# Optimization experiments

Hardware: AMD Instinct MI355X
Metric: run time of the kernel (lower is better)

## Reference

```python
import jax, jax.numpy as jnp
import numpy as np

C = 4  # n_features_per_level
RES = [128, 256, 512, 1024]  # base_resolution=128, per_level_scale=2, n_levels=4


def grid_sample(grid, pts):
    """Bilinear grid_sample, align_corners=False, zero padding.
    grid: (B, C, H, W); pts: (B, N, 2) with pts[...,0]=x (width), pts[...,1]=y (height).
    Returns (B, C, N)."""
    B, Cc, H, W = grid.shape
    fx = (pts[..., 0] + 1.0) * 0.5 * W - 0.5
    fy = (pts[..., 1] + 1.0) * 0.5 * H - 0.5
    x0 = jnp.floor(fx)
    y0 = jnp.floor(fy)
    wx = (fx - x0)[:, None, :]
    wy = (fy - y0)[:, None, :]
    x0 = x0.astype(jnp.int32)
    y0 = y0.astype(jnp.int32)

    def corner(xi, yi):
        valid = ((xi >= 0) & (xi < W) & (yi >= 0) & (yi < H)).astype(grid.dtype)
        xc = jnp.clip(xi, 0, W - 1)
        yc = jnp.clip(yi, 0, H - 1)
        vals = jax.vmap(lambda g, yy, xx: g[:, yy, xx])(grid, yc, xc)  # (B, C, N)
        return vals * valid[:, None, :]

    v00 = corner(x0, y0)
    v10 = corner(x0 + 1, y0)
    v01 = corner(x0, y0 + 1)
    v11 = corner(x0 + 1, y0 + 1)
    return (v00 * (1 - wx) * (1 - wy) + v10 * wx * (1 - wy)
            + v01 * (1 - wx) * wy + v11 * wx * wy)


def _flat(f):
    # (3, C, N) -> (N, 3*C), matching torch out.reshape(3*C, N).T
    return f.reshape(3 * f.shape[1], f.shape[2]).T


def _forward(x, triplanes, trilines):
    x2 = x * 2.0 - 1.0  # map [0,1] -> [-1,1]
    # plane projections: (xz), (yx), (zy)
    x_pl = jnp.stack([
        jnp.stack([x2[:, 0], x2[:, 2]], -1),
        jnp.stack([x2[:, 1], x2[:, 0]], -1),
        jnp.stack([x2[:, 2], x2[:, 1]], -1)], 0)  # (3, N, 2)
    x_li = jnp.stack([x2[:, 0], x2[:, 1], x2[:, 2]], 0)
    x_li = jnp.stack([x_li, jnp.zeros_like(x_li)], -1)  # (3, N, 2)
    feats = []
    for tp, tl in zip(triplanes, trilines):
        f = _flat(grid_sample(tp, x_pl)) * _flat(grid_sample(tl, x_li))  # (N, 3C)
        feats.append(f)
    return jnp.concatenate(feats, -1)  # (N, 3*C*n_levels)


def setup_inputs() -> dict:
    key = jax.random.key(0)
    ks = jax.random.split(key, 9)
    N = 1 << 20
    d = {"x": jax.random.uniform(ks[0], (N, 3), jnp.float32)}
    for i, r in enumerate(RES):
        d[f"triplane_{i}"] = jax.random.normal(ks[1 + i], (3, C, r, r), jnp.float32)
        d[f"triline_{i}"] = jax.random.normal(ks[5 + i], (3, C, r, 1), jnp.float32)
    return d


def reference(x, triplane_0, triplane_1, triplane_2, triplane_3,
              triline_0, triline_1, triline_2, triline_3):
    triplanes = [triplane_0, triplane_1, triplane_2, triplane_3]
    trilines = [triline_0, triline_1, triline_2, triline_3]
    return _forward(x, triplanes, trilines)
```

## Files before the change

kernel.cpp:

```cpp
#include <hip/hip_runtime.h>
#include <cstdint>


static constexpr int LVL_OFF[4] = {0, 196608, 983040, 4128768};
static constexpr int S_OFF = 16711680;
static constexpr size_t WS_NEED = (size_t)(S_OFF + 48) * sizeof(float);

__global__ __launch_bounds__(256) void repack_lvl(const float* __restrict__ src,
                                                  float* __restrict__ dst,
                                                  int rr_shift ) {
    int j = blockIdx.x * blockDim.x + threadIdx.x;
    int c  = j & 3;
    int t  = j >> 2;
    int p  = t >> rr_shift;
    int yx = t & ((1 << rr_shift) - 1);
    dst[j] = src[(((size_t)(p * 4 + c)) << rr_shift) + yx];
}

__global__ void line_consts(const float* __restrict__ tl0, const float* __restrict__ tl1,
                            const float* __restrict__ tl2, const float* __restrict__ tl3,
                            float* __restrict__ s_out) {
    int i = threadIdx.x;
    if (i >= 48) return;
    int l = i / 12, rem = i % 12, p = rem >> 2, c = rem & 3;
    const float* tl = (l == 0) ? tl0 : (l == 1) ? tl1 : (l == 2) ? tl2 : tl3;
    int r = 128 << l;
    const float* row = tl + (size_t)((p << 2) + c) * r;
    int y0 = (r >> 1) - 1;
    s_out[i] = 0.5f * row[y0] + 0.5f * row[y0 + 1];
}

struct BilinW {
    int i00, i10, i01, i11;
    float w00, w10, w01, w11;
};

__device__ __forceinline__ BilinW bilin_weights(int r, float u, float v) {
    float fr = (float)r;
    float fx = (u + 1.0f) * 0.5f * fr - 0.5f;
    float fy = (v + 1.0f) * 0.5f * fr - 0.5f;
    float x0f = floorf(fx), y0f = floorf(fy);
    float wx = fx - x0f, wy = fy - y0f;
    int x0 = (int)x0f, y0 = (int)y0f;
    int x1 = x0 + 1, y1 = y0 + 1;
    float vx0 = ((unsigned)x0 < (unsigned)r) ? 1.0f : 0.0f;
    float vx1 = ((unsigned)x1 < (unsigned)r) ? 1.0f : 0.0f;
    float vy0 = ((unsigned)y0 < (unsigned)r) ? 1.0f : 0.0f;
    float vy1 = ((unsigned)y1 < (unsigned)r) ? 1.0f : 0.0f;
    int x0c = min(max(x0, 0), r - 1), x1c = min(max(x1, 0), r - 1);
    int y0c = min(max(y0, 0), r - 1), y1c = min(max(y1, 0), r - 1);
    BilinW b;
    b.i00 = y0c * r + x0c; b.i10 = y0c * r + x1c;
    b.i01 = y1c * r + x0c; b.i11 = y1c * r + x1c;
    b.w00 = (1.0f - wx) * (1.0f - wy) * vx0 * vy0;
    b.w10 = wx * (1.0f - wy) * vx1 * vy0;
    b.w01 = (1.0f - wx) * wy * vx0 * vy1;
    b.w11 = wx * wy * vx1 * vy1;
    return b;
}

__device__ __forceinline__ float line_w(float t) {
    float fx = (t + 1.0f) * 0.5f - 0.5f;
    float x0f = floorf(fx);
    float wx = fx - x0f;
    int x0 = (int)x0f;
    float w = 0.0f;
    if (x0 == 0) w += 1.0f - wx;
    if (x0 == -1) w += wx;
    return w;
}

template <bool VEC4OUT>
__global__ __launch_bounds__(256) void tri_main(const float* __restrict__ x,
                                                const float4* __restrict__ planes,
                                                const float* __restrict__ S,
                                                float* __restrict__ out, int N) {
    int n = blockIdx.x * blockDim.x + threadIdx.x;
    if (n >= N) return;
    float ax = x[n * 3 + 0] * 2.0f - 1.0f;
    float ay = x[n * 3 + 1] * 2.0f - 1.0f;
    float az = x[n * 3 + 2] * 2.0f - 1.0f;
    const float U[3] = {ax, ay, az};
    const float V[3] = {az, ax, ay};
    const float LW[3] = {line_w(ax), line_w(ay), line_w(az)};

#pragma unroll
    for (int l = 0; l < 4; ++l) {
        const int r = 128 << l;
#pragma unroll
        for (int p = 0; p < 3; ++p) {
            const float4* G = planes + (LVL_OFF[l] >> 2) + (size_t)p * r * r;
            BilinW b = bilin_weights(r, U[p], V[p]);
            float4 g00 = G[b.i00], g10 = G[b.i10], g01 = G[b.i01], g11 = G[b.i11];
            float w = LW[p];
            float sx = S[(l * 3 + p) * 4 + 0] * w;
            float sy = S[(l * 3 + p) * 4 + 1] * w;
            float sz = S[(l * 3 + p) * 4 + 2] * w;
            float sw = S[(l * 3 + p) * 4 + 3] * w;
            float4 o;
            o.x = (g00.x * b.w00 + g10.x * b.w10 + g01.x * b.w01 + g11.x * b.w11) * sx;
            o.y = (g00.y * b.w00 + g10.y * b.w10 + g01.y * b.w01 + g11.y * b.w11) * sy;
            o.z = (g00.z * b.w00 + g10.z * b.w10 + g01.z * b.w01 + g11.z * b.w11) * sz;
            o.w = (g00.w * b.w00 + g10.w * b.w10 + g01.w * b.w01 + g11.w * b.w11) * sw;
            size_t base = (size_t)n * 48 + (size_t)(l * 12 + p * 4);
            if (VEC4OUT) {
                *reinterpret_cast<float4*>(out + base) = o;
            } else {
                out[base + 0] = o.x; out[base + 1] = o.y;
                out[base + 2] = o.z; out[base + 3] = o.w;
            }
        }
    }
}

__global__ __launch_bounds__(256) void tri_direct(
        const float* __restrict__ x,
        const float* __restrict__ tp0, const float* __restrict__ tp1,
        const float* __restrict__ tp2, const float* __restrict__ tp3,
        const float* __restrict__ tl0, const float* __restrict__ tl1,
        const float* __restrict__ tl2, const float* __restrict__ tl3,
        float* __restrict__ out, int N) {
    int n = blockIdx.x * blockDim.x + threadIdx.x;
    if (n >= N) return;
    float ax = x[n * 3 + 0] * 2.0f - 1.0f;
    float ay = x[n * 3 + 1] * 2.0f - 1.0f;
    float az = x[n * 3 + 2] * 2.0f - 1.0f;
    const float U[3] = {ax, ay, az};
    const float V[3] = {az, ax, ay};
    const float LW[3] = {line_w(ax), line_w(ay), line_w(az)};
    const float* TP[4] = {tp0, tp1, tp2, tp3};
    const float* TL[4] = {tl0, tl1, tl2, tl3};

#pragma unroll
    for (int l = 0; l < 4; ++l) {
        const int r = 128 << l;
        const int rr = r * r;
        const int y0 = (r >> 1) - 1;
#pragma unroll
        for (int p = 0; p < 3; ++p) {
            const float* G = TP[l] + (size_t)(p * 4) * rr;
            BilinW b = bilin_weights(r, U[p], V[p]);
            const float w = LW[p];
#pragma unroll
            for (int c = 0; c < 4; ++c) {
                const float* Gc = G + (size_t)c * rr;
                float acc = Gc[b.i00] * b.w00 + Gc[b.i10] * b.w10 +
                            Gc[b.i01] * b.w01 + Gc[b.i11] * b.w11;
                const float* row = TL[l] + (size_t)((p << 2) + c) * r;
                float s = 0.5f * row[y0] + 0.5f * row[y0 + 1];
                out[(size_t)n * 48 + l * 12 + p * 4 + c] = acc * (s * w);
            }
        }
    }
}

extern "C" void kernel_launch(void* const* d_in, const int* in_sizes, int n_in,
                              void* d_out, int out_size, void* d_ws, size_t ws_size,
                              hipStream_t stream) {
    const float* x = (const float*)d_in[0];
    const float* tp[4];
    const float* tl[4];
    bool interleaved = (n_in >= 9) && (in_sizes[2] == 1536);
    for (int l = 0; l < 4; ++l) {
        if (interleaved) {
            tp[l] = (const float*)d_in[1 + 2 * l];
            tl[l] = (const float*)d_in[2 + 2 * l];
        } else {
            tp[l] = (const float*)d_in[1 + l];
            tl[l] = (const float*)d_in[5 + l];
        }
    }
    int N = in_sizes[0] / 3;
    float* out = (float*)d_out;
    int grid = (N + 255) / 256;

    bool ws_ok = (ws_size >= WS_NEED) && (((uintptr_t)d_ws & 15u) == 0);
    if (ws_ok) {
        float* ws = (float*)d_ws;
        for (int l = 0; l < 4; ++l) {
            int r = 128 << l;
            int total = 12 * r * r;
            int rr_shift = 2 * (7 + l);
            repack_lvl<<<total / 256, 256, 0, stream>>>(tp[l], ws + LVL_OFF[l], rr_shift);
        }
        line_consts<<<1, 64, 0, stream>>>(tl[0], tl[1], tl[2], tl[3], ws + S_OFF);
        if (((uintptr_t)d_out & 15u) == 0) {
            tri_main<true><<<grid, 256, 0, stream>>>(x, (const float4*)ws, ws + S_OFF, out, N);
        } else {
            tri_main<false><<<grid, 256, 0, stream>>>(x, (const float4*)ws, ws + S_OFF, out, N);
        }
    } else {
        tri_direct<<<grid, 256, 0, stream>>>(
            x, tp[0], tp[1], tp[2], tp[3], tl[0], tl[1], tl[2], tl[3], out, N);
    }
}
```

Measured before the change: 660.4 us.

## Merge repack kernels and split per-point work across four level threads

Replaces the four per-level repack launches and the line-constant kernel with a single repack_all kernel. Each thread of that kernel gathers four channels and writes one float4. The main kernel now assigns one thread per (point, level) pair instead of one per point. Each thread issues all 12 plane gathers up front and writes its 48 output bytes with nontemporal vector stores, which should give more memory-level parallelism and fewer launches. In exchange, every thread recomputes the input load and line weights, and the grid is four times larger.

```diff
diff --git a/kernel.cpp b/kernel.cpp
--- a/kernel.cpp
+++ b/kernel.cpp
@@ -1,33 +1,44 @@
 #include <hip/hip_runtime.h>
 #include <cstdint>
 
+
+typedef float f32x4 __attribute__((ext_vector_type(4)));
 
 static constexpr int LVL_OFF[4] = {0, 196608, 983040, 4128768};
 static constexpr int S_OFF = 16711680;
 static constexpr size_t WS_NEED = (size_t)(S_OFF + 48) * sizeof(float);
-
-__global__ __launch_bounds__(256) void repack_lvl(const float* __restrict__ src,
-                                                  float* __restrict__ dst,
-                                                  int rr_shift ) {
-    int j = blockIdx.x * blockDim.x + threadIdx.x;
-    int c  = j & 3;
-    int t  = j >> 2;
-    int p  = t >> rr_shift;
-    int yx = t & ((1 << rr_shift) - 1);
-    dst[j] = src[(((size_t)(p * 4 + c)) << rr_shift) + yx];
-}
-
-__global__ void line_consts(const float* __restrict__ tl0, const float* __restrict__ tl1,
-                            const float* __restrict__ tl2, const float* __restrict__ tl3,
-                            float* __restrict__ s_out) {
-    int i = threadIdx.x;
-    if (i >= 48) return;
-    int l = i / 12, rem = i % 12, p = rem >> 2, c = rem & 3;
-    const float* tl = (l == 0) ? tl0 : (l == 1) ? tl1 : (l == 2) ? tl2 : tl3;
-    int r = 128 << l;
-    const float* row = tl + (size_t)((p << 2) + c) * r;
-    int y0 = (r >> 1) - 1;
-    s_out[i] = 0.5f * row[y0] + 0.5f * row[y0 + 1];
+static constexpr int TEXELS = 4177920;
+
+__global__ __launch_bounds__(256) void repack_all(
+        const float* __restrict__ tp0, const float* __restrict__ tp1,
+        const float* __restrict__ tp2, const float* __restrict__ tp3,
+        const float* __restrict__ tl0, const float* __restrict__ tl1,
+        const float* __restrict__ tl2, const float* __restrict__ tl3,
+        float* __restrict__ ws) {
+    int t = blockIdx.x * 256 + threadIdx.x;
+    const float* src; int rr_shift, texoff;
+    if (t < 49152)        { src = tp0; rr_shift = 14; texoff = 0; }
+    else if (t < 245760)  { src = tp1; rr_shift = 16; texoff = 49152; }
+    else if (t < 1032192) { src = tp2; rr_shift = 18; texoff = 245760; }
+    else                  { src = tp3; rr_shift = 20; texoff = 1032192; }
+    int local = t - texoff;
+    int p  = local >> rr_shift;
+    int yx = local & ((1 << rr_shift) - 1);
+    const float* s0 = src + ((size_t)(p << 2) << rr_shift) + yx;
+    float4 o;
+    o.x = s0[0];
+    o.y = s0[(size_t)1 << rr_shift];
+    o.z = s0[(size_t)2 << rr_shift];
+    o.w = s0[(size_t)3 << rr_shift];
+    reinterpret_cast<float4*>(ws)[t] = o;
+    if (t < 48) {
+        int ll = t / 12, rem = t % 12, pp = rem >> 2, cc = rem & 3;
+        const float* tl = (ll == 0) ? tl0 : (ll == 1) ? tl1 : (ll == 2) ? tl2 : tl3;
+        int r = 128 << ll;
+        const float* row = tl + (size_t)((pp << 2) + cc) * r;
+        int y0 = (r >> 1) - 1;
+        ws[S_OFF + t] = 0.5f * row[y0] + 0.5f * row[y0 + 1];
+    }
 }
 
 struct BilinW {
@@ -70,46 +81,61 @@
     return w;
 }
 
+__device__ __forceinline__ f32x4 bacc(const float4& A, const float4& B2,
+                                      const float4& C2, const float4& D,
+                                      const BilinW& b, const float4& s, float lw) {
+    f32x4 o;
+    o.x = (A.x * b.w00 + B2.x * b.w10 + C2.x * b.w01 + D.x * b.w11) * (s.x * lw);
+    o.y = (A.y * b.w00 + B2.y * b.w10 + C2.y * b.w01 + D.y * b.w11) * (s.y * lw);
+    o.z = (A.z * b.w00 + B2.z * b.w10 + C2.z * b.w01 + D.z * b.w11) * (s.z * lw);
+    o.w = (A.w * b.w00 + B2.w * b.w10 + C2.w * b.w01 + D.w * b.w11) * (s.w * lw);
+    return o;
+}
+
 template <bool VEC4OUT>
-__global__ __launch_bounds__(256) void tri_main(const float* __restrict__ x,
-                                                const float4* __restrict__ planes,
-                                                const float* __restrict__ S,
-                                                float* __restrict__ out, int N) {
-    int n = blockIdx.x * blockDim.x + threadIdx.x;
+__global__ __launch_bounds__(256, 2) void tri_split4(
+        const float* __restrict__ x, const float4* __restrict__ planes,
+        const float* __restrict__ S, float* __restrict__ out, int N) {
+    int gid = blockIdx.x * 256 + threadIdx.x;
+    int n = gid >> 2;
+    int l = gid & 3;
     if (n >= N) return;
     float ax = x[n * 3 + 0] * 2.0f - 1.0f;
     float ay = x[n * 3 + 1] * 2.0f - 1.0f;
     float az = x[n * 3 + 2] * 2.0f - 1.0f;
-    const float U[3] = {ax, ay, az};
-    const float V[3] = {az, ax, ay};
-    const float LW[3] = {line_w(ax), line_w(ay), line_w(az)};
-
-#pragma unroll
-    for (int l = 0; l < 4; ++l) {
-        const int r = 128 << l;
-#pragma unroll
-        for (int p = 0; p < 3; ++p) {
-            const float4* G = planes + (LVL_OFF[l] >> 2) + (size_t)p * r * r;
-            BilinW b = bilin_weights(r, U[p], V[p]);
-            float4 g00 = G[b.i00], g10 = G[b.i10], g01 = G[b.i01], g11 = G[b.i11];
-            float w = LW[p];
-            float sx = S[(l * 3 + p) * 4 + 0] * w;
-            float sy = S[(l * 3 + p) * 4 + 1] * w;
-            float sz = S[(l * 3 + p) * 4 + 2] * w;
-            float sw = S[(l * 3 + p) * 4 + 3] * w;
-            float4 o;
-            o.x = (g00.x * b.w00 + g10.x * b.w10 + g01.x * b.w01 + g11.x * b.w11) * sx;
-            o.y = (g00.y * b.w00 + g10.y * b.w10 + g01.y * b.w01 + g11.y * b.w11) * sy;
-            o.z = (g00.z * b.w00 + g10.z * b.w10 + g01.z * b.w01 + g11.z * b.w11) * sz;
-            o.w = (g00.w * b.w00 + g10.w * b.w10 + g01.w * b.w01 + g11.w * b.w11) * sw;
-            size_t base = (size_t)n * 48 + (size_t)(l * 12 + p * 4);
-            if (VEC4OUT) {
-                *reinterpret_cast<float4*>(out + base) = o;
-            } else {
-                out[base + 0] = o.x; out[base + 1] = o.y;
-                out[base + 2] = o.z; out[base + 3] = o.w;
-            }
-        }
+    const int r = 128 << l;
+    const int rr = r * r;
+    int texoff = (l == 0) ? 0 : (l == 1) ? 49152 : (l == 2) ? 245760 : 1032192;
+    const float4* G0 = planes + texoff;
+    const float4* G1 = G0 + rr;
+    const float4* G2 = G1 + rr;
+    BilinW b0 = bilin_weights(r, ax, az);
+    BilinW b1 = bilin_weights(r, ay, ax);
+    BilinW b2 = bilin_weights(r, az, ay);
+    float4 g0a = G0[b0.i00], g0b = G0[b0.i10], g0c = G0[b0.i01], g0d = G0[b0.i11];
+    float4 g1a = G1[b1.i00], g1b = G1[b1.i10], g1c = G1[b1.i01], g1d = G1[b1.i11];
+    float4 g2a = G2[b2.i00], g2b = G2[b2.i10], g2c = G2[b2.i01], g2d = G2[b2.i11];
+    float lw0 = line_w(ax), lw1 = line_w(ay), lw2 = line_w(az);
+    const float4* S4 = reinterpret_cast<const float4*>(S);
+    float4 s0 = S4[l * 3 + 0], s1 = S4[l * 3 + 1], s2 = S4[l * 3 + 2];
+
+    f32x4 o0 = bacc(g0a, g0b, g0c, g0d, b0, s0, lw0);
+    f32x4 o1 = bacc(g1a, g1b, g1c, g1d, b1, s1, lw1);
+    f32x4 o2 = bacc(g2a, g2b, g2c, g2d, b2, s2, lw2);
+
+    size_t base = (size_t)n * 48 + (size_t)l * 12;
+    if (VEC4OUT) {
+        f32x4* op = reinterpret_cast<f32x4*>(out + base);
+        __builtin_nontemporal_store(o0, op);
+        __builtin_nontemporal_store(o1, op + 1);
+        __builtin_nontemporal_store(o2, op + 2);
+    } else {
+        out[base + 0] = o0.x; out[base + 1]  = o0.y;
+        out[base + 2] = o0.z; out[base + 3]  = o0.w;
+        out[base + 4] = o1.x; out[base + 5]  = o1.y;
+        out[base + 6] = o1.z; out[base + 7]  = o1.w;
+        out[base + 8] = o2.x; out[base + 9]  = o2.y;
+        out[base + 10] = o2.z; out[base + 11] = o2.w;
     }
 }
 
@@ -172,24 +198,23 @@
     }
     int N = in_sizes[0] / 3;
     float* out = (float*)d_out;
-    int grid = (N + 255) / 256;
 
     bool ws_ok = (ws_size >= WS_NEED) && (((uintptr_t)d_ws & 15u) == 0);
     if (ws_ok) {
         float* ws = (float*)d_ws;
-        for (int l = 0; l < 4; ++l) {
-            int r = 128 << l;
-            int total = 12 * r * r;
-            int rr_shift = 2 * (7 + l);
-            repack_lvl<<<total / 256, 256, 0, stream>>>(tp[l], ws + LVL_OFF[l], rr_shift);
-        }
-        line_consts<<<1, 64, 0, stream>>>(tl[0], tl[1], tl[2], tl[3], ws + S_OFF);
+        repack_all<<<TEXELS / 256, 256, 0, stream>>>(
+            tp[0], tp[1], tp[2], tp[3], tl[0], tl[1], tl[2], tl[3], ws);
+        long long total = 4LL * N;
+        int grid = (int)((total + 255) / 256);
         if (((uintptr_t)d_out & 15u) == 0) {
-            tri_main<true><<<grid, 256, 0, stream>>>(x, (const float4*)ws, ws + S_OFF, out, N);
+            tri_split4<true><<<grid, 256, 0, stream>>>(
+                x, (const float4*)ws, ws + S_OFF, out, N);
         } else {
-            tri_main<false><<<grid, 256, 0, stream>>>(x, (const float4*)ws, ws + S_OFF, out, N);
+            tri_split4<false><<<grid, 256, 0, stream>>>(
+                x, (const float4*)ws, ws + S_OFF, out, N);
         }
     } else {
+        int grid = (N + 255) / 256;
         tri_direct<<<grid, 256, 0, stream>>>(
             x, tp[0], tp[1], tp[2], tp[3], tl[0], tl[1], tl[2], tl[3], out, N);
     }
```

Result: faster. 621.4 us (-5.9%).
